# Kernel tuning notes

Measured on AMD Instinct MI355X. Metric: run time of the kernel, lower is better.

## Reference

```python
import jax, jax.numpy as jnp
import numpy as np

B, NQ, NK, D, H, DR, MLPD = 32, 32, 4096, 256, 8, 2, 2048
ID = D // DR  # internal dim for downsampled cross-attention
EPS = 1e-5


def _ln(x, g, b):
    m = jnp.mean(x, -1, keepdims=True)
    v = jnp.mean((x - m) ** 2, -1, keepdims=True)
    return (x - m) / jnp.sqrt(v + EPS) * g + b


def _attn(q, k, v, qw, qb, kw, kb, vw, vb, ow, ob):
    # linear projections (weights stored as [in, out])
    q = q @ qw + qb
    k = k @ kw + kb
    v = v @ vw + vb
    b, nq, c = q.shape
    d = c // H
    qh = q.reshape(b, nq, H, d)
    kh = k.reshape(b, -1, H, d)
    vh = v.reshape(b, -1, H, d)
    scores = jnp.einsum('bqhd,bkhd->bhqk', qh, kh) * (1.0 / np.sqrt(d))
    a = jax.nn.softmax(scores, axis=-1)
    o = jnp.einsum('bhqk,bkhd->bqhd', a, vh).reshape(b, nq, c)
    return o @ ow + ob


def _forward(queries, keys, query_pe,
             sa_qw, sa_qb, sa_kw, sa_kb, sa_vw, sa_vb, sa_ow, sa_ob,
             t2i_qw, t2i_qb, t2i_kw, t2i_kb, t2i_vw, t2i_vb, t2i_ow, t2i_ob,
             i2t_qw, i2t_qb, i2t_kw, i2t_kb, i2t_vw, i2t_vb, i2t_ow, i2t_ob,
             mlp_w1, mlp_b1, mlp_w2, mlp_b2,
             ln1_g, ln1_b, ln2_g, ln2_b, ln3_g, ln3_b, ln4_g, ln4_b):
    # skip_first_layer_pe = False
    queries = queries + query_pe
    attn_out = _attn(queries, queries, queries,
                     sa_qw, sa_qb, sa_kw, sa_kb, sa_vw, sa_vb, sa_ow, sa_ob)
    queries = _ln(queries + attn_out, ln1_g, ln1_b)
    # cross attention: tokens -> image
    q = queries + query_pe
    attn_out = _attn(q, keys, keys,
                     t2i_qw, t2i_qb, t2i_kw, t2i_kb, t2i_vw, t2i_vb, t2i_ow, t2i_ob)
    queries = _ln(queries + attn_out, ln2_g, ln2_b)
    # MLP block (num_layers=1): act(x W1 + b1) W2 + b2, act = ReLU
    mlp_out = jax.nn.relu(queries @ mlp_w1 + mlp_b1) @ mlp_w2 + mlp_b2
    queries = _ln(queries + mlp_out, ln3_g, ln3_b)
    # cross attention: image -> tokens
    q = queries + query_pe
    attn_out = _attn(keys, q, queries,
                     i2t_qw, i2t_qb, i2t_kw, i2t_kb, i2t_vw, i2t_vb, i2t_ow, i2t_ob)
    keys = _ln(keys + attn_out, ln4_g, ln4_b)
    return queries, keys


def setup_inputs() -> dict:
    key = jax.random.key(0)
    ks = iter(jax.random.split(key, 64))
    def w(shape, s=0.02):
        return jax.random.normal(next(ks), shape, jnp.float32) * s
    inp = {
        'queries': w((B, NQ, D), 1.0),
        'keys': w((B, NK, D), 1.0),
        'query_pe': w((B, NQ, D), 1.0),
    }
    for pre, idim in [('sa', D), ('t2i', ID), ('i2t', ID)]:
        inp[pre + '_qw'] = w((D, idim)); inp[pre + '_qb'] = jnp.zeros((idim,), jnp.float32)
        inp[pre + '_kw'] = w((D, idim)); inp[pre + '_kb'] = jnp.zeros((idim,), jnp.float32)
        inp[pre + '_vw'] = w((D, idim)); inp[pre + '_vb'] = jnp.zeros((idim,), jnp.float32)
        inp[pre + '_ow'] = w((idim, D)); inp[pre + '_ob'] = jnp.zeros((D,), jnp.float32)
    inp['mlp_w1'] = w((D, MLPD)); inp['mlp_b1'] = jnp.zeros((MLPD,), jnp.float32)
    inp['mlp_w2'] = w((MLPD, D)); inp['mlp_b2'] = jnp.zeros((D,), jnp.float32)
    for i in range(1, 5):
        inp['ln%d_g' % i] = jnp.ones((D,), jnp.float32)
        inp['ln%d_b' % i] = jnp.zeros((D,), jnp.float32)
    return inp


def reference(queries, keys, query_pe,
              sa_qw, sa_qb, sa_kw, sa_kb, sa_vw, sa_vb, sa_ow, sa_ob,
              t2i_qw, t2i_qb, t2i_kw, t2i_kb, t2i_vw, t2i_vb, t2i_ow, t2i_ob,
              i2t_qw, i2t_qb, i2t_kw, i2t_kb, i2t_vw, i2t_vb, i2t_ow, i2t_ob,
              mlp_w1, mlp_b1, mlp_w2, mlp_b2,
              ln1_g, ln1_b, ln2_g, ln2_b, ln3_g, ln3_b, ln4_g, ln4_b):
    return _forward(queries, keys, query_pe,
                    sa_qw, sa_qb, sa_kw, sa_kb, sa_vw, sa_vb, sa_ow, sa_ob,
                    t2i_qw, t2i_qb, t2i_kw, t2i_kb, t2i_vw, t2i_vb, t2i_ow, t2i_ob,
                    i2t_qw, i2t_qb, i2t_kw, i2t_kb, i2t_vw, i2t_vb, i2t_ow, i2t_ob,
                    mlp_w1, mlp_b1, mlp_w2, mlp_b2,
                    ln1_g, ln1_b, ln2_g, ln2_b, ln3_g, ln3_b, ln4_g, ln4_b)
```

## Files before the change

kernel.cpp:

```cpp
#include <hip/hip_runtime.h>

typedef unsigned short u16;
typedef __attribute__((ext_vector_type(8))) short s16x8;
typedef __attribute__((ext_vector_type(4))) float f32x4;
typedef __attribute__((ext_vector_type(8))) unsigned short u16x8;

__device__ __forceinline__ float b2f(u16 u) {
  union { unsigned int i; float f; } v; v.i = ((unsigned int)u) << 16; return v.f;
}
__device__ __forceinline__ u16 f2b(float f) {
  union { float f; unsigned int i; } v; v.f = f;
  unsigned int r = v.i + 0x7FFFu + ((v.i >> 16) & 1u);
  return (u16)(r >> 16);
}
__device__ __forceinline__ int pk2(float a, float b) {
  return (int)f2b(a) | ((int)f2b(b) << 16);
}

template<bool RELU>
__global__ void __launch_bounds__(256) k_gemm(
    const u16* __restrict__ A, const u16* __restrict__ Wt,
    const float* __restrict__ bias, u16* __restrict__ C, int N, int K)
{
  __shared__ int4 smem4[2048];
  char* AsB = (char*)smem4;
  char* WsB = (char*)smem4 + 16384;
  const int t = threadIdx.x;
  const int lane = t & 63, wid = t >> 6;
  const int wm = wid >> 1, wn = wid & 1;
  const int l16 = lane & 15, lhi = lane >> 4;
  const int bCol = blockIdx.x * 128;
  const int bRow = blockIdx.y * 128;

  f32x4 acc[4][4];
#pragma unroll
  for (int i = 0; i < 4; ++i)
#pragma unroll
    for (int j = 0; j < 4; ++j) acc[i][j] = (f32x4){0.f, 0.f, 0.f, 0.f};

  const int nk = K >> 6;
  for (int kt = 0; kt < nk; ++kt) {
    const int k0 = kt << 6;
    int4 av[4], wv[4];
#pragma unroll
    for (int i = 0; i < 4; ++i) {
      int L = i * 4096 + t * 16;
      int r = L >> 7, cl = (L >> 4) & 7;
      av[i] = *(const int4*)(A + (size_t)(bRow + r) * K + k0 + cl * 8);
      wv[i] = *(const int4*)(Wt + (size_t)(bCol + r) * K + k0 + cl * 8);
    }
    if (kt) __syncthreads();
#pragma unroll
    for (int i = 0; i < 4; ++i) {
      int L = i * 4096 + t * 16;
      int r = L >> 7, cl = (L >> 4) & 7;
      int off = r * 128 + ((cl ^ (r & 7)) << 4);
      *(int4*)(AsB + off) = av[i];
      *(int4*)(WsB + off) = wv[i];
    }
    __syncthreads();
#pragma unroll
    for (int kk = 0; kk < 2; ++kk) {
      s16x8 af[4], bfr[4];
#pragma unroll
      for (int mt = 0; mt < 4; ++mt) {
        int r = wm * 64 + mt * 16 + l16;
        int ch = kk * 4 + lhi;
        af[mt] = *(const s16x8*)(AsB + r * 128 + ((ch ^ (r & 7)) << 4));
      }
#pragma unroll
      for (int nt = 0; nt < 4; ++nt) {
        int r = wn * 64 + nt * 16 + l16;
        int ch = kk * 4 + lhi;
        bfr[nt] = *(const s16x8*)(WsB + r * 128 + ((ch ^ (r & 7)) << 4));
      }
#pragma unroll
      for (int mt = 0; mt < 4; ++mt)
#pragma unroll
        for (int nt = 0; nt < 4; ++nt)
          acc[mt][nt] = __builtin_amdgcn_mfma_f32_16x16x32_bf16(
              af[mt], bfr[nt], acc[mt][nt], 0, 0, 0);
    }
  }
#pragma unroll
  for (int mt = 0; mt < 4; ++mt) {
#pragma unroll
    for (int nt = 0; nt < 4; ++nt) {
      int cg = bCol + wn * 64 + nt * 16 + l16;
      float bv = bias[cg];
#pragma unroll
      for (int rg = 0; rg < 4; ++rg) {
        int rgl = bRow + wm * 64 + mt * 16 + lhi * 4 + rg;
        float v = acc[mt][nt][rg] + bv;
        if (RELU) v = fmaxf(v, 0.f);
        C[(size_t)rgl * N + cg] = f2b(v);
      }
    }
  }
}

__global__ void __launch_bounds__(512, 2) k_gemm_kvq(
    const float* __restrict__ A, const u16* __restrict__ Wt,
    const float* __restrict__ bias, u16* __restrict__ KV, u16* __restrict__ QB)
{
  __shared__ char smem[49152];
  char* AsB = smem;
  const int t = threadIdx.x;
  const int lane = t & 63, wid = t >> 6;
  const int wm = wid >> 2, wn = wid & 3;
  const int l16 = lane & 15, lhi = lane >> 4;
  const int bRow = blockIdx.x * 128;

  f32x4 acc[4][6];
#pragma unroll
  for (int i = 0; i < 4; ++i)
#pragma unroll
    for (int j = 0; j < 6; ++j) acc[i][j] = (f32x4){0.f, 0.f, 0.f, 0.f};

  for (int kt = 0; kt < 4; ++kt) {
    const int k0 = kt << 6;
    float4 a0r[2], a1r[2];
#pragma unroll
    for (int i = 0; i < 2; ++i) {
      int L = i * 8192 + t * 16;
      int r = L >> 7, cl = (L >> 4) & 7;
      const float* Af = A + (size_t)(bRow + r) * 256 + k0 + cl * 8;
      a0r[i] = *(const float4*)Af;
      a1r[i] = *(const float4*)(Af + 4);
    }
    if (kt) __syncthreads();
#pragma unroll
    for (int i = 0; i < 2; ++i) {
      int L = i * 8192 + t * 16;
      int r = L >> 7, cl = (L >> 4) & 7;
      int4 p = (int4){pk2(a0r[i].x, a0r[i].y), pk2(a0r[i].z, a0r[i].w),
                      pk2(a1r[i].x, a1r[i].y), pk2(a1r[i].z, a1r[i].w)};
      *(int4*)(AsB + r * 128 + ((cl ^ (r & 7)) << 4)) = p;
    }
    __syncthreads();
#pragma unroll
    for (int kk = 0; kk < 2; ++kk) {
      s16x8 af[4], bfr[6];
#pragma unroll
      for (int nt = 0; nt < 6; ++nt) {
        int row = wn * 96 + nt * 16 + l16;
        bfr[nt] = *(const s16x8*)(Wt + (size_t)row * 256 + k0 + kk * 32 + lhi * 8);
      }
#pragma unroll
      for (int mt = 0; mt < 4; ++mt) {
        int r = wm * 64 + mt * 16 + l16;
        int ch = kk * 4 + lhi;
        af[mt] = *(const s16x8*)(AsB + r * 128 + ((ch ^ (r & 7)) << 4));
      }
#pragma unroll
      for (int mt = 0; mt < 4; ++mt)
#pragma unroll
        for (int nt = 0; nt < 6; ++nt)
          acc[mt][nt] = __builtin_amdgcn_mfma_f32_16x16x32_bf16(
              af[mt], bfr[nt], acc[mt][nt], 0, 0, 0);
    }
  }
  u16* ldsO = (u16*)smem;
  for (int half = 0; half < 2; ++half) {
    __syncthreads();
    if (wm == half) {
#pragma unroll
      for (int mt = 0; mt < 4; ++mt) {
#pragma unroll
        for (int nt = 0; nt < 6; ++nt) {
          int cg = wn * 96 + nt * 16 + l16;
          float bv = bias[cg];
#pragma unroll
          for (int rg = 0; rg < 4; ++rg) {
            int r = mt * 16 + lhi * 4 + rg;
            ldsO[r * 384 + cg] = f2b(acc[mt][nt][rg] + bv);
          }
        }
      }
    }
    __syncthreads();
#pragma unroll
    for (int i = 0; i < 6; ++i) {
      int chunk = i * 512 + t;
      int r = chunk / 48, c8 = chunk - r * 48;
      int row = bRow + half * 64 + r;
      int4 v = *(int4*)(ldsO + r * 384 + c8 * 8);
      if (c8 < 32) *(int4*)(KV + (size_t)row * 256 + c8 * 8) = v;
      else         *(int4*)(QB + (size_t)row * 128 + (c8 - 32) * 8) = v;
    }
  }
}

__global__ void __launch_bounds__(256) k_gemm_ln(
    const u16* __restrict__ A, const u16* __restrict__ Wt,
    const float* __restrict__ bias, const float* __restrict__ res,
    const float* __restrict__ g, const float* __restrict__ bl,
    float* __restrict__ out)
{
  __shared__ int4 smem4[512];
  __shared__ float rsum[2][32][2], rsq[2][32][2];
  char* AsB = (char*)smem4;
  const int t = threadIdx.x;
  const int lane = t & 63, wid = t >> 6;
  const int wm = wid >> 1, wn = wid & 1;
  const int l16 = lane & 15, lhi = lane >> 4;
  const int bRow = blockIdx.x * 64;

  f32x4 acc[2][8];
#pragma unroll
  for (int i = 0; i < 2; ++i)
#pragma unroll
    for (int j = 0; j < 8; ++j) acc[i][j] = (f32x4){0.f, 0.f, 0.f, 0.f};

  for (int kt = 0; kt < 2; ++kt) {
    const int k0 = kt << 6;
    int4 av[2];
#pragma unroll
    for (int i = 0; i < 2; ++i) {
      int L = i * 4096 + t * 16;
      int r = L >> 7, cl = (L >> 4) & 7;
      av[i] = *(const int4*)(A + (size_t)(bRow + r) * 128 + k0 + cl * 8);
    }
    if (kt) __syncthreads();
#pragma unroll
    for (int i = 0; i < 2; ++i) {
      int L = i * 4096 + t * 16;
      int r = L >> 7, cl = (L >> 4) & 7;
      *(int4*)(AsB + r * 128 + ((cl ^ (r & 7)) << 4)) = av[i];
    }
    __syncthreads();
#pragma unroll
    for (int kk = 0; kk < 2; ++kk) {
      s16x8 af[2], bfr[8];
#pragma unroll
      for (int nt = 0; nt < 8; ++nt) {
        int row = wn * 128 + nt * 16 + l16;
        bfr[nt] = *(const s16x8*)(Wt + (size_t)row * 128 + k0 + kk * 32 + lhi * 8);
      }
#pragma unroll
      for (int mt = 0; mt < 2; ++mt) {
        int r = wm * 32 + mt * 16 + l16;
        int ch = kk * 4 + lhi;
        af[mt] = *(const s16x8*)(AsB + r * 128 + ((ch ^ (r & 7)) << 4));
      }
#pragma unroll
      for (int mt = 0; mt < 2; ++mt)
#pragma unroll
        for (int nt = 0; nt < 8; ++nt)
          acc[mt][nt] = __builtin_amdgcn_mfma_f32_16x16x32_bf16(
              af[mt], bfr[nt], acc[mt][nt], 0, 0, 0);
    }
  }
#pragma unroll
  for (int mt = 0; mt < 2; ++mt) {
#pragma unroll
    for (int nt = 0; nt < 8; ++nt) {
      int cg = wn * 128 + nt * 16 + l16;
      float bv = bias[cg];
#pragma unroll
      for (int rg = 0; rg < 4; ++rg) {
        int row = bRow + wm * 32 + mt * 16 + lhi * 4 + rg;
        acc[mt][nt][rg] += bv + res[(size_t)row * 256 + cg];
      }
    }
  }
#pragma unroll
  for (int mt = 0; mt < 2; ++mt) {
#pragma unroll
    for (int rg = 0; rg < 4; ++rg) {
      float ps = 0.f, pq = 0.f;
#pragma unroll
      for (int nt = 0; nt < 8; ++nt) {
        float v = acc[mt][nt][rg];
        ps += v; pq += v * v;
      }
#pragma unroll
      for (int msk = 1; msk < 16; msk <<= 1) {
        ps += __shfl_xor(ps, msk);
        pq += __shfl_xor(pq, msk);
      }
      if (l16 == 0) {
        int rl = mt * 16 + lhi * 4 + rg;
        rsum[wm][rl][wn] = ps;
        rsq[wm][rl][wn] = pq;
      }
    }
  }
  __syncthreads();
#pragma unroll
  for (int mt = 0; mt < 2; ++mt) {
#pragma unroll
    for (int rg = 0; rg < 4; ++rg) {
      int rl = mt * 16 + lhi * 4 + rg;
      float ts = rsum[wm][rl][0] + rsum[wm][rl][1];
      float tq = rsq[wm][rl][0] + rsq[wm][rl][1];
      float mean = ts * (1.f / 256.f);
      float var = tq * (1.f / 256.f) - mean * mean;
      float rstd = rsqrtf(var + 1e-5f);
      int row = bRow + wm * 32 + rl;
#pragma unroll
      for (int nt = 0; nt < 8; ++nt) {
        int cg = wn * 128 + nt * 16 + l16;
        out[(size_t)row * 256 + cg] =
            (acc[mt][nt][rg] - mean) * rstd * g[cg] + bl[cg];
      }
    }
  }
}

struct TDesc { const float* src; void* dst; int K; int N; int mode; int blk0; };
struct TArgs { TDesc d[24]; int n; };

__global__ void __launch_bounds__(256) k_trans(TArgs a)
{
  int blk = blockIdx.x;
  int i = 0;
  while (i + 1 < a.n && blk >= a.d[i + 1].blk0) ++i;
  TDesc td = a.d[i];
  int e = (blk - td.blk0) * 256 + threadIdx.x;
  int tot = td.K * td.N;
  if (e >= tot) return;
  if (td.mode == 0) {
    int k = e / td.N, n = e - k * td.N;
    ((u16*)td.dst)[(size_t)n * td.K + k] = f2b(td.src[e]);
  } else {
    ((float*)td.dst)[e] = td.src[e];
  }
}

__global__ void __launch_bounds__(256) k_addpe(
    const float* __restrict__ q, const float* __restrict__ pe,
    float* __restrict__ outf, u16* __restrict__ outb)
{
  int i = blockIdx.x * 256 + threadIdx.x;
  float v = q[i] + pe[i];
  outf[i] = v;
  outb[i] = f2b(v);
}

__global__ void __launch_bounds__(64) k_attn_sa(
    const u16* __restrict__ QKV, u16* __restrict__ out)
{
  __shared__ float Q[32][33], K[32][33], V[32][33];
  int b = blockIdx.x >> 3, h = blockIdx.x & 7;
  int t = threadIdx.x;
  for (int idx = t; idx < 1024; idx += 64) {
    int i = idx >> 5, d = idx & 31;
    size_t base = (size_t)(b * 32 + i) * 768 + h * 32 + d;
    Q[i][d] = b2f(QKV[base]);
    K[i][d] = b2f(QKV[base + 256]);
    V[i][d] = b2f(QKV[base + 512]);
  }
  __syncthreads();
  int i = t & 31, half = t >> 5;
  float s[16];
#pragma unroll
  for (int jj = 0; jj < 16; ++jj) {
    int j = half * 16 + jj;
    float a = 0.f;
#pragma unroll
    for (int d = 0; d < 32; ++d) a += Q[i][d] * K[j][d];
    s[jj] = a * 0.17677669529663687f;
  }
  float m = s[0];
#pragma unroll
  for (int jj = 1; jj < 16; ++jj) m = fmaxf(m, s[jj]);
  m = fmaxf(m, __shfl_xor(m, 32));
  float sum = 0.f;
#pragma unroll
  for (int jj = 0; jj < 16; ++jj) { s[jj] = __expf(s[jj] - m); sum += s[jj]; }
  sum += __shfl_xor(sum, 32);
  float o[32];
#pragma unroll
  for (int d = 0; d < 32; ++d) o[d] = 0.f;
#pragma unroll
  for (int jj = 0; jj < 16; ++jj) {
    int j = half * 16 + jj;
    float p = s[jj];
#pragma unroll
    for (int d = 0; d < 32; ++d) o[d] += p * V[j][d];
  }
  float inv = 1.f / sum;
#pragma unroll
  for (int d = 0; d < 32; ++d) {
    float v = o[d] + __shfl_xor(o[d], 32);
    if (half == 0) out[(size_t)(b * 32 + i) * 256 + h * 32 + d] = f2b(v * inv);
  }
}

__global__ void __launch_bounds__(128) k_attn_t2i_part(
    const u16* __restrict__ Qt, const u16* __restrict__ KV,
    float* __restrict__ part)
{
  __shared__ int4 kvs[4096];
  int c = blockIdx.x, b = blockIdx.y;
  int tid = threadIdx.x;
  const int4* src = (const int4*)(KV + ((size_t)b * 4096 + c * 128) * 256);
  for (int i = tid; i < 4096; i += 128) kvs[i] = src[i];
  __syncthreads();
  int qp = tid >> 3, h = tid & 7;
  const u16* lds = (const u16*)kvs;

  float q0[16], q1[16];
  {
    const u16* p0 = Qt + (size_t)(b * 32 + qp) * 128 + h * 16;
    const u16* p1 = Qt + (size_t)(b * 32 + qp + 16) * 128 + h * 16;
    u16x8 a0 = *(const u16x8*)p0, b0 = *(const u16x8*)(p0 + 8);
    u16x8 a1 = *(const u16x8*)p1, b1 = *(const u16x8*)(p1 + 8);
#pragma unroll
    for (int e = 0; e < 8; ++e) {
      q0[e] = b2f(a0[e]); q0[8 + e] = b2f(b0[e]);
      q1[e] = b2f(a1[e]); q1[8 + e] = b2f(b1[e]);
    }
  }
  float m0 = -INFINITY, s0 = 0.f, m1 = -INFINITY, s1 = 0.f;
  float acc0[16], acc1[16];
#pragma unroll
  for (int d = 0; d < 16; ++d) { acc0[d] = 0.f; acc1[d] = 0.f; }

  for (int j = 0; j < 128; ++j) {
    const u16* kr = lds + j * 256 + h * 16;
    u16x8 ka = *(const u16x8*)kr;
    u16x8 kb = *(const u16x8*)(kr + 8);
    float l0 = 0.f, l1 = 0.f;
#pragma unroll
    for (int e = 0; e < 8; ++e) {
      float klo = b2f(ka[e]), khi = b2f(kb[e]);
      l0 += q0[e] * klo + q0[8 + e] * khi;
      l1 += q1[e] * klo + q1[8 + e] * khi;
    }
    l0 *= 0.25f; l1 *= 0.25f;
    const u16* vr = kr + 128;
    u16x8 va = *(const u16x8*)vr;
    u16x8 vb = *(const u16x8*)(vr + 8);
    float nm0 = fmaxf(m0, l0), nm1 = fmaxf(m1, l1);
    float c0 = __expf(m0 - nm0), p0 = __expf(l0 - nm0);
    float c1 = __expf(m1 - nm1), p1 = __expf(l1 - nm1);
    s0 = s0 * c0 + p0; s1 = s1 * c1 + p1;
#pragma unroll
    for (int e = 0; e < 8; ++e) {
      float vlo = b2f(va[e]), vhi = b2f(vb[e]);
      acc0[e] = acc0[e] * c0 + p0 * vlo;
      acc0[8 + e] = acc0[8 + e] * c0 + p0 * vhi;
      acc1[e] = acc1[e] * c1 + p1 * vlo;
      acc1[8 + e] = acc1[8 + e] * c1 + p1 * vhi;
    }
    m0 = nm0; m1 = nm1;
  }
  float* r0 = part + (((size_t)(b * 32 + qp) * 8 + h) * 32 + c) * 18;
  float* r1 = part + (((size_t)(b * 32 + qp + 16) * 8 + h) * 32 + c) * 18;
#pragma unroll
  for (int d = 0; d < 16; ++d) { r0[d] = acc0[d]; r1[d] = acc1[d]; }
  r0[16] = m0; r0[17] = s0;
  r1[16] = m1; r1[17] = s1;
}

__global__ void __launch_bounds__(256) k_attn_t2i_merge(
    const float* __restrict__ part, u16* __restrict__ out)
{
  int b = blockIdx.x >> 3, h = blockIdx.x & 7;
  int q = threadIdx.x >> 3, ds = threadIdx.x & 7;
  const float* base = part + (((size_t)(b * 32 + q) * 8 + h) * 32) * 18;
  float mg = -INFINITY;
#pragma unroll 4
  for (int c = 0; c < 32; ++c) mg = fmaxf(mg, base[c * 18 + 16]);
  float sg = 0.f, a0 = 0.f, a1 = 0.f;
#pragma unroll 4
  for (int c = 0; c < 32; ++c) {
    const float* rec = base + c * 18;
    float w = __expf(rec[16] - mg);
    sg += rec[17] * w;
    a0 += rec[ds * 2] * w;
    a1 += rec[ds * 2 + 1] * w;
  }
  float inv = 1.f / sg;
  u16* op = out + (size_t)(b * 32 + q) * 128 + h * 16 + ds * 2;
  op[0] = f2b(a0 * inv);
  op[1] = f2b(a1 * inv);
}

__global__ void __launch_bounds__(256) k_attn_i2t(
    const u16* __restrict__ Qb, const u16* __restrict__ Kc,
    const u16* __restrict__ Vc, u16* __restrict__ out)
{
  __shared__ float Kl[32][132], Vl[32][132];
  int blk = blockIdx.x;
  int b = blk >> 7;
  int r0 = (blk & 127) * 32;
  for (int idx = threadIdx.x; idx < 4096; idx += 256) {
    int j = idx >> 7, c = idx & 127;
    Kl[j][c] = b2f(Kc[(size_t)(b * 32 + j) * 128 + c]);
    Vl[j][c] = b2f(Vc[(size_t)(b * 32 + j) * 128 + c]);
  }
  __syncthreads();
  int lr = threadIdx.x >> 3, h = threadIdx.x & 7;
  size_t row = (size_t)b * 4096 + r0 + lr;
  const u16* qp = Qb + row * 128 + h * 16;
  float q[16];
  {
    u16x8 qa = *(const u16x8*)qp;
    u16x8 qb2 = *(const u16x8*)(qp + 8);
#pragma unroll
    for (int e = 0; e < 8; ++e) { q[e] = b2f(qa[e]); q[8 + e] = b2f(qb2[e]); }
  }
  float lg[32];
  float mx = -INFINITY;
#pragma unroll
  for (int j = 0; j < 32; ++j) {
    float a = 0.f;
#pragma unroll
    for (int d = 0; d < 16; ++d) a += q[d] * Kl[j][h * 16 + d];
    lg[j] = a * 0.25f;
    mx = fmaxf(mx, lg[j]);
  }
  float sum = 0.f;
#pragma unroll
  for (int j = 0; j < 32; ++j) { lg[j] = __expf(lg[j] - mx); sum += lg[j]; }
  float acc[16];
#pragma unroll
  for (int d = 0; d < 16; ++d) acc[d] = 0.f;
#pragma unroll
  for (int j = 0; j < 32; ++j) {
    float p = lg[j];
#pragma unroll
    for (int d = 0; d < 16; ++d) acc[d] += p * Vl[j][h * 16 + d];
  }
  float inv = 1.f / sum;
  u16* op = out + row * 128 + h * 16;
#pragma unroll
  for (int d = 0; d < 16; ++d) op[d] = f2b(acc[d] * inv);
}

__global__ void __launch_bounds__(256) k_addln_small(
    const float* __restrict__ res, const u16* __restrict__ delta,
    const float* __restrict__ g, const float* __restrict__ bb,
    float* outf, u16* outb, const float* pe, u16* outpe)
{
  int row = blockIdx.x * 4 + (threadIdx.x >> 6);
  int lane = threadIdx.x & 63;
  size_t base = (size_t)row * 256 + lane * 4;
  float4 xv = *(const float4*)(res + base);
  ushort4 dv = *(const ushort4*)(delta + base);
  float v0 = xv.x + b2f(dv.x), v1 = xv.y + b2f(dv.y);
  float v2 = xv.z + b2f(dv.z), v3 = xv.w + b2f(dv.w);
  float sum = v0 + v1 + v2 + v3;
  float sq = v0 * v0 + v1 * v1 + v2 * v2 + v3 * v3;
#pragma unroll
  for (int msk = 1; msk < 64; msk <<= 1) {
    sum += __shfl_xor(sum, msk);
    sq += __shfl_xor(sq, msk);
  }
  float mean = sum * (1.f / 256.f);
  float var = sq * (1.f / 256.f) - mean * mean;
  float rstd = rsqrtf(var + 1e-5f);
  float4 gv = *(const float4*)(g + lane * 4);
  float4 bv = *(const float4*)(bb + lane * 4);
  float y0 = (v0 - mean) * rstd * gv.x + bv.x;
  float y1 = (v1 - mean) * rstd * gv.y + bv.y;
  float y2 = (v2 - mean) * rstd * gv.z + bv.z;
  float y3 = (v3 - mean) * rstd * gv.w + bv.w;
  if (outf) { float4 o{y0, y1, y2, y3}; *(float4*)(outf + base) = o; }
  if (outb) {
    ushort4 o{f2b(y0), f2b(y1), f2b(y2), f2b(y3)};
    *(ushort4*)(outb + base) = o;
  }
  if (outpe) {
    float4 pv = *(const float4*)(pe + base);
    ushort4 o{f2b(y0 + pv.x), f2b(y1 + pv.y), f2b(y2 + pv.z), f2b(y3 + pv.w)};
    *(ushort4*)(outpe + base) = o;
  }
}

extern "C" void kernel_launch(void* const* d_in, const int* in_sizes, int n_in,
                              void* d_out, int out_size, void* d_ws, size_t ws_size,
                              hipStream_t stream)
{
  (void)in_sizes; (void)n_in; (void)out_size; (void)ws_size;
  const float* queries = (const float*)d_in[0];
  const float* keys    = (const float*)d_in[1];
  const float* qpe     = (const float*)d_in[2];
  const float* sa_qw = (const float*)d_in[3];  const float* sa_qb = (const float*)d_in[4];
  const float* sa_kw = (const float*)d_in[5];  const float* sa_kb = (const float*)d_in[6];
  const float* sa_vw = (const float*)d_in[7];  const float* sa_vb = (const float*)d_in[8];
  const float* sa_ow = (const float*)d_in[9];  const float* sa_ob = (const float*)d_in[10];
  const float* t2i_qw = (const float*)d_in[11]; const float* t2i_qb = (const float*)d_in[12];
  const float* t2i_kw = (const float*)d_in[13]; const float* t2i_kb = (const float*)d_in[14];
  const float* t2i_vw = (const float*)d_in[15]; const float* t2i_vb = (const float*)d_in[16];
  const float* t2i_ow = (const float*)d_in[17]; const float* t2i_ob = (const float*)d_in[18];
  const float* i2t_qw = (const float*)d_in[19]; const float* i2t_qb = (const float*)d_in[20];
  const float* i2t_kw = (const float*)d_in[21]; const float* i2t_kb = (const float*)d_in[22];
  const float* i2t_vw = (const float*)d_in[23]; const float* i2t_vb = (const float*)d_in[24];
  const float* i2t_ow = (const float*)d_in[25]; const float* i2t_ob = (const float*)d_in[26];
  const float* mlp_w1 = (const float*)d_in[27]; const float* mlp_b1 = (const float*)d_in[28];
  const float* mlp_w2 = (const float*)d_in[29]; const float* mlp_b2 = (const float*)d_in[30];
  const float* ln1_g = (const float*)d_in[31]; const float* ln1_b = (const float*)d_in[32];
  const float* ln2_g = (const float*)d_in[33]; const float* ln2_b = (const float*)d_in[34];
  const float* ln3_g = (const float*)d_in[35]; const float* ln3_b = (const float*)d_in[36];
  const float* ln4_g = (const float*)d_in[37]; const float* ln4_b = (const float*)d_in[38];

  float* out_q = (float*)d_out;
  float* out_k = out_q + 262144;

  u16* kvbuf  = (u16*)out_k;
  u16* qb_big = (u16*)out_k + 33554432;
  float* t2i_part = (float*)((u16*)out_k + 50331648);

  char* ws = (char*)d_ws;
  size_t off = 0;
  auto alloc = [&](size_t bytes) -> char* {
    char* p = ws + off;
    off += (bytes + 255) & ~(size_t)255;
    return p;
  };
  u16* wt_saqkv = (u16*)alloc(768 * 256 * 2);
  u16* wt_saow  = (u16*)alloc(256 * 256 * 2);
  u16* wt_t2iq  = (u16*)alloc(128 * 256 * 2);
  u16* wt_kvq   = (u16*)alloc(384 * 256 * 2);
  u16* wt_t2io  = (u16*)alloc(256 * 128 * 2);
  u16* wt_i2tk  = (u16*)alloc(128 * 256 * 2);
  u16* wt_i2tv  = (u16*)alloc(128 * 256 * 2);
  u16* wt_i2to  = (u16*)alloc(256 * 128 * 2);
  u16* wt_w1    = (u16*)alloc(2048 * 256 * 2);
  u16* wt_w2    = (u16*)alloc(256 * 2048 * 2);
  float* b_saqkv = (float*)alloc(768 * 4);
  float* b_kvq   = (float*)alloc(384 * 4);
  float* q0f = (float*)alloc(262144 * 4);
  float* q1f = (float*)alloc(262144 * 4);
  float* q2f = (float*)alloc(262144 * 4);
  u16* q0b   = (u16*)alloc(262144 * 2);
  u16* qkvs  = (u16*)alloc(786432 * 2);
  u16* attn1 = (u16*)alloc(262144 * 2);
  u16* o1    = (u16*)alloc(262144 * 2);
  u16* q1pe  = (u16*)alloc(262144 * 2);
  u16* qt    = (u16*)alloc(131072 * 2);
  u16* at2   = (u16*)alloc(131072 * 2);
  u16* o2    = (u16*)alloc(262144 * 2);
  u16* q2b   = (u16*)alloc(262144 * 2);
  u16* hbuf  = (u16*)alloc(2097152 * 2);
  u16* mo    = (u16*)alloc(262144 * 2);
  u16* q3b   = (u16*)alloc(262144 * 2);
  u16* q3pe  = (u16*)alloc(262144 * 2);
  u16* kc    = (u16*)alloc(131072 * 2);
  u16* vc    = (u16*)alloc(131072 * 2);
  u16* ab_big = (u16*)alloc((size_t)16777216 * 2);

  TArgs ta{};
  int nb = 0, id = 0;
  auto addT = [&](const float* s, void* d, int K, int N, int mode) {
    ta.d[id].src = s; ta.d[id].dst = d; ta.d[id].K = K; ta.d[id].N = N;
    ta.d[id].mode = mode; ta.d[id].blk0 = nb;
    nb += (K * N + 255) / 256;
    ++id;
  };
  addT(sa_qw, wt_saqkv, 256, 256, 0);
  addT(sa_kw, wt_saqkv + 256 * 256, 256, 256, 0);
  addT(sa_vw, wt_saqkv + 512 * 256, 256, 256, 0);
  addT(sa_ow, wt_saow, 256, 256, 0);
  addT(t2i_qw, wt_t2iq, 256, 128, 0);
  addT(t2i_kw, wt_kvq, 256, 128, 0);
  addT(t2i_vw, wt_kvq + 128 * 256, 256, 128, 0);
  addT(i2t_qw, wt_kvq + 256 * 256, 256, 128, 0);
  addT(t2i_ow, wt_t2io, 128, 256, 0);
  addT(i2t_kw, wt_i2tk, 256, 128, 0);
  addT(i2t_vw, wt_i2tv, 256, 128, 0);
  addT(i2t_ow, wt_i2to, 128, 256, 0);
  addT(mlp_w1, wt_w1, 256, 2048, 0);
  addT(mlp_w2, wt_w2, 2048, 256, 0);
  addT(sa_qb, b_saqkv, 1, 256, 1);
  addT(sa_kb, b_saqkv + 256, 1, 256, 1);
  addT(sa_vb, b_saqkv + 512, 1, 256, 1);
  addT(t2i_kb, b_kvq, 1, 128, 1);
  addT(t2i_vb, b_kvq + 128, 1, 128, 1);
  addT(i2t_qb, b_kvq + 256, 1, 128, 1);
  ta.n = id;
  k_trans<<<nb, 256, 0, stream>>>(ta);

  k_addpe<<<1024, 256, 0, stream>>>(queries, qpe, q0f, q0b);
  k_gemm<false><<<dim3(6, 8), 256, 0, stream>>>(q0b, wt_saqkv, b_saqkv,
                                                qkvs, 768, 256);
  k_attn_sa<<<256, 64, 0, stream>>>(qkvs, attn1);
  k_gemm<false><<<dim3(2, 8), 256, 0, stream>>>(attn1, wt_saow, sa_ob,
                                                o1, 256, 256);
  k_addln_small<<<256, 256, 0, stream>>>(q0f, o1, ln1_g, ln1_b, q1f, nullptr,
                                         qpe, q1pe);
  k_gemm<false><<<dim3(1, 8), 256, 0, stream>>>(q1pe, wt_t2iq, t2i_qb,
                                                qt, 128, 256);
  k_gemm_kvq<<<1024, 512, 0, stream>>>(keys, wt_kvq, b_kvq, kvbuf, qb_big);
  k_attn_t2i_part<<<dim3(32, 32), 128, 0, stream>>>(qt, kvbuf, t2i_part);
  k_attn_t2i_merge<<<256, 256, 0, stream>>>(t2i_part, at2);
  k_gemm<false><<<dim3(2, 8), 256, 0, stream>>>(at2, wt_t2io, t2i_ob,
                                                o2, 256, 128);
  k_addln_small<<<256, 256, 0, stream>>>(q1f, o2, ln2_g, ln2_b, q2f, q2b,
                                         nullptr, nullptr);
  k_gemm<true><<<dim3(16, 8), 256, 0, stream>>>(q2b, wt_w1, mlp_b1,
                                                hbuf, 2048, 256);
  k_gemm<false><<<dim3(2, 8), 256, 0, stream>>>(hbuf, wt_w2, mlp_b2,
                                                mo, 256, 2048);
  k_addln_small<<<256, 256, 0, stream>>>(q2f, mo, ln3_g, ln3_b, out_q, q3b,
                                         qpe, q3pe);
  k_gemm<false><<<dim3(1, 8), 256, 0, stream>>>(q3pe, wt_i2tk, i2t_kb,
                                                kc, 128, 256);
  k_gemm<false><<<dim3(1, 8), 256, 0, stream>>>(q3b, wt_i2tv, i2t_vb,
                                                vc, 128, 256);
  k_attn_i2t<<<4096, 256, 0, stream>>>(qb_big, kc, vc, ab_big);
  k_gemm_ln<<<2048, 256, 0, stream>>>(ab_big, wt_i2to, i2t_ob, keys,
                                      ln4_g, ln4_b, out_k);
}
```

Measured before the change: 574.0 us.

## Fuse query-side self-attention, out-proj, LayerNorm and t2i Q projection into one kernel

Replaces six launches (add-PE, QKV GEMM, self-attention, out-proj GEMM, add+LayerNorm, t2i Q GEMM) with one kernel that has one block per batch and keeps intermediates in LDS. This removes launch overhead and global round-trips for the small query-side tensors. The trade-off is only 32 blocks on the GPU, with each block streaming all the weights from global/L2, so parallelism is lower. LayerNorm now uses a single-pass variance (E[x^2]-mean^2).

```diff
diff --git a/kernel.cpp b/kernel.cpp
--- a/kernel.cpp
+++ b/kernel.cpp
@@ -96,6 +96,239 @@
         C[(size_t)rgl * N + cg] = f2b(v);
       }
     }
+  }
+}
+
+__global__ void __launch_bounds__(256) k_qphase1(
+    const float* __restrict__ queries, const float* __restrict__ qpe,
+    const u16* __restrict__ Wqkv,
+    const float* __restrict__ bqkv,
+    const u16* __restrict__ Wo,
+    const float* __restrict__ ob,
+    const float* __restrict__ g1, const float* __restrict__ b1,
+    const u16* __restrict__ Wq2,
+    const float* __restrict__ qb2,
+    float* __restrict__ q1f, u16* __restrict__ qt)
+{
+  __shared__ float q0f[32][260];
+  __shared__ u16 qkv[32][776];
+  __shared__ u16 atb[32][264];
+  __shared__ float rs[32][4], rq[32][4];
+  const int b = blockIdx.x;
+  const int t = threadIdx.x;
+  const int lane = t & 63, w = t >> 6;
+  const int l16 = lane & 15, lhi = lane >> 4;
+
+  {
+    const float4* qg = (const float4*)(queries + (size_t)b * 8192);
+    const float4* pg = (const float4*)(qpe + (size_t)b * 8192);
+    for (int i = t; i < 2048; i += 256) {
+      int row = i >> 6, c4 = (i & 63) * 4;
+      float4 qv = qg[i], pv = pg[i];
+      *(float4*)&q0f[row][c4] =
+          (float4){qv.x + pv.x, qv.y + pv.y, qv.z + pv.z, qv.w + pv.w};
+    }
+  }
+  __syncthreads();
+
+  {
+    f32x4 acc[2][12];
+#pragma unroll
+    for (int i = 0; i < 2; ++i)
+#pragma unroll
+      for (int j = 0; j < 12; ++j) acc[i][j] = (f32x4){0.f, 0.f, 0.f, 0.f};
+#pragma unroll
+    for (int kk = 0; kk < 8; ++kk) {
+      const int ko = kk * 32 + lhi * 8;
+      s16x8 af[2], bfr[12];
+#pragma unroll
+      for (int mt = 0; mt < 2; ++mt) {
+        const float* ap = &q0f[mt * 16 + l16][ko];
+        float4 x = *(const float4*)ap;
+        float4 y = *(const float4*)(ap + 4);
+        int4 p = (int4){pk2(x.x, x.y), pk2(x.z, x.w),
+                        pk2(y.x, y.y), pk2(y.z, y.w)};
+        af[mt] = *(s16x8*)&p;
+      }
+#pragma unroll
+      for (int nt = 0; nt < 12; ++nt) {
+        int row = w * 192 + nt * 16 + l16;
+        bfr[nt] = *(const s16x8*)(Wqkv + (size_t)row * 256 + ko);
+      }
+#pragma unroll
+      for (int mt = 0; mt < 2; ++mt)
+#pragma unroll
+        for (int nt = 0; nt < 12; ++nt)
+          acc[mt][nt] = __builtin_amdgcn_mfma_f32_16x16x32_bf16(
+              af[mt], bfr[nt], acc[mt][nt], 0, 0, 0);
+    }
+#pragma unroll
+    for (int mt = 0; mt < 2; ++mt)
+#pragma unroll
+      for (int nt = 0; nt < 12; ++nt) {
+        int cg = w * 192 + nt * 16 + l16;
+        float bv = bqkv[cg];
+#pragma unroll
+        for (int rg = 0; rg < 4; ++rg)
+          qkv[mt * 16 + lhi * 4 + rg][cg] = f2b(acc[mt][nt][rg] + bv);
+      }
+  }
+  __syncthreads();
+
+  {
+    int q = t >> 3, h = t & 7;
+    float Qh[32];
+#pragma unroll
+    for (int c = 0; c < 4; ++c) {
+      u16x8 v = *(const u16x8*)&qkv[q][h * 32 + c * 8];
+#pragma unroll
+      for (int e = 0; e < 8; ++e) Qh[c * 8 + e] = b2f(v[e]);
+    }
+    float s[32], mx = -INFINITY;
+#pragma unroll 4
+    for (int j = 0; j < 32; ++j) {
+      float a = 0.f;
+#pragma unroll
+      for (int c = 0; c < 4; ++c) {
+        u16x8 v = *(const u16x8*)&qkv[j][256 + h * 32 + c * 8];
+#pragma unroll
+        for (int e = 0; e < 8; ++e) a += Qh[c * 8 + e] * b2f(v[e]);
+      }
+      s[j] = a * 0.17677669529663687f;
+      mx = fmaxf(mx, s[j]);
+    }
+    float sum = 0.f;
+#pragma unroll
+    for (int j = 0; j < 32; ++j) { s[j] = __expf(s[j] - mx); sum += s[j]; }
+    float o[32];
+#pragma unroll
+    for (int d = 0; d < 32; ++d) o[d] = 0.f;
+#pragma unroll 4
+    for (int j = 0; j < 32; ++j) {
+      float p = s[j];
+#pragma unroll
+      for (int c = 0; c < 4; ++c) {
+        u16x8 v = *(const u16x8*)&qkv[j][512 + h * 32 + c * 8];
+#pragma unroll
+        for (int e = 0; e < 8; ++e) o[c * 8 + e] += p * b2f(v[e]);
+      }
+    }
+    float inv = 1.f / sum;
+#pragma unroll
+    for (int d = 0; d < 32; ++d) atb[q][h * 32 + d] = f2b(o[d] * inv);
+  }
+  __syncthreads();
+
+  float yv[2][4][4];
+  {
+    f32x4 acc[2][4];
+#pragma unroll
+    for (int i = 0; i < 2; ++i)
+#pragma unroll
+      for (int j = 0; j < 4; ++j) acc[i][j] = (f32x4){0.f, 0.f, 0.f, 0.f};
+#pragma unroll
+    for (int kk = 0; kk < 8; ++kk) {
+      const int ko = kk * 32 + lhi * 8;
+      s16x8 af[2], bfr[4];
+#pragma unroll
+      for (int mt = 0; mt < 2; ++mt)
+        af[mt] = *(const s16x8*)&atb[mt * 16 + l16][ko];
+#pragma unroll
+      for (int nt = 0; nt < 4; ++nt) {
+        int row = w * 64 + nt * 16 + l16;
+        bfr[nt] = *(const s16x8*)(Wo + (size_t)row * 256 + ko);
+      }
+#pragma unroll
+      for (int mt = 0; mt < 2; ++mt)
+#pragma unroll
+        for (int nt = 0; nt < 4; ++nt)
+          acc[mt][nt] = __builtin_amdgcn_mfma_f32_16x16x32_bf16(
+              af[mt], bfr[nt], acc[mt][nt], 0, 0, 0);
+    }
+#pragma unroll
+    for (int mt = 0; mt < 2; ++mt) {
+#pragma unroll
+      for (int rg = 0; rg < 4; ++rg) {
+        int row = mt * 16 + lhi * 4 + rg;
+        float ps = 0.f, pq = 0.f;
+#pragma unroll
+        for (int nt = 0; nt < 4; ++nt) {
+          int cg = w * 64 + nt * 16 + l16;
+          float v = acc[mt][nt][rg] + ob[cg] + q0f[row][cg];
+          yv[mt][nt][rg] = v;
+          ps += v; pq += v * v;
+        }
+#pragma unroll
+        for (int msk = 1; msk < 16; msk <<= 1) {
+          ps += __shfl_xor(ps, msk);
+          pq += __shfl_xor(pq, msk);
+        }
+        if (l16 == 0) { rs[row][w] = ps; rq[row][w] = pq; }
+      }
+    }
+  }
+  __syncthreads();
+  {
+#pragma unroll
+    for (int mt = 0; mt < 2; ++mt) {
+#pragma unroll
+      for (int rg = 0; rg < 4; ++rg) {
+        int row = mt * 16 + lhi * 4 + rg;
+        float ts = rs[row][0] + rs[row][1] + rs[row][2] + rs[row][3];
+        float tq = rq[row][0] + rq[row][1] + rq[row][2] + rq[row][3];
+        float mean = ts * (1.f / 256.f);
+        float var = tq * (1.f / 256.f) - mean * mean;
+        float rstd = rsqrtf(var + 1e-5f);
+#pragma unroll
+        for (int nt = 0; nt < 4; ++nt) {
+          int cg = w * 64 + nt * 16 + l16;
+          float y = (yv[mt][nt][rg] - mean) * rstd * g1[cg] + b1[cg];
+          size_t gi = ((size_t)b * 32 + row) * 256 + cg;
+          q1f[gi] = y;
+          atb[row][cg] = f2b(y + qpe[gi]);
+        }
+      }
+    }
+  }
+  __syncthreads();
+
+  {
+    f32x4 acc[2][2];
+#pragma unroll
+    for (int i = 0; i < 2; ++i)
+#pragma unroll
+      for (int j = 0; j < 2; ++j) acc[i][j] = (f32x4){0.f, 0.f, 0.f, 0.f};
+#pragma unroll
+    for (int kk = 0; kk < 8; ++kk) {
+      const int ko = kk * 32 + lhi * 8;
+      s16x8 af[2], bfr[2];
+#pragma unroll
+      for (int mt = 0; mt < 2; ++mt)
+        af[mt] = *(const s16x8*)&atb[mt * 16 + l16][ko];
+#pragma unroll
+      for (int nt = 0; nt < 2; ++nt) {
+        int row = w * 32 + nt * 16 + l16;
+        bfr[nt] = *(const s16x8*)(Wq2 + (size_t)row * 256 + ko);
+      }
+#pragma unroll
+      for (int mt = 0; mt < 2; ++mt)
+#pragma unroll
+        for (int nt = 0; nt < 2; ++nt)
+          acc[mt][nt] = __builtin_amdgcn_mfma_f32_16x16x32_bf16(
+              af[mt], bfr[nt], acc[mt][nt], 0, 0, 0);
+    }
+#pragma unroll
+    for (int mt = 0; mt < 2; ++mt)
+#pragma unroll
+      for (int nt = 0; nt < 2; ++nt) {
+        int cg = w * 32 + nt * 16 + l16;
+        float bv = qb2[cg];
+#pragma unroll
+        for (int rg = 0; rg < 4; ++rg) {
+          int row = mt * 16 + lhi * 4 + rg;
+          qt[((size_t)b * 32 + row) * 128 + cg] = f2b(acc[mt][nt][rg] + bv);
+        }
+      }
   }
 }
 
@@ -325,66 +558,6 @@
     ((u16*)td.dst)[(size_t)n * td.K + k] = f2b(td.src[e]);
   } else {
     ((float*)td.dst)[e] = td.src[e];
-  }
-}
-
-__global__ void __launch_bounds__(256) k_addpe(
-    const float* __restrict__ q, const float* __restrict__ pe,
-    float* __restrict__ outf, u16* __restrict__ outb)
-{
-  int i = blockIdx.x * 256 + threadIdx.x;
-  float v = q[i] + pe[i];
-  outf[i] = v;
-  outb[i] = f2b(v);
-}
-
-__global__ void __launch_bounds__(64) k_attn_sa(
-    const u16* __restrict__ QKV, u16* __restrict__ out)
-{
-  __shared__ float Q[32][33], K[32][33], V[32][33];
-  int b = blockIdx.x >> 3, h = blockIdx.x & 7;
-  int t = threadIdx.x;
-  for (int idx = t; idx < 1024; idx += 64) {
-    int i = idx >> 5, d = idx & 31;
-    size_t base = (size_t)(b * 32 + i) * 768 + h * 32 + d;
-    Q[i][d] = b2f(QKV[base]);
-    K[i][d] = b2f(QKV[base + 256]);
-    V[i][d] = b2f(QKV[base + 512]);
-  }
-  __syncthreads();
-  int i = t & 31, half = t >> 5;
-  float s[16];
-#pragma unroll
-  for (int jj = 0; jj < 16; ++jj) {
-    int j = half * 16 + jj;
-    float a = 0.f;
-#pragma unroll
-    for (int d = 0; d < 32; ++d) a += Q[i][d] * K[j][d];
-    s[jj] = a * 0.17677669529663687f;
-  }
-  float m = s[0];
-#pragma unroll
-  for (int jj = 1; jj < 16; ++jj) m = fmaxf(m, s[jj]);
-  m = fmaxf(m, __shfl_xor(m, 32));
-  float sum = 0.f;
-#pragma unroll
-  for (int jj = 0; jj < 16; ++jj) { s[jj] = __expf(s[jj] - m); sum += s[jj]; }
-  sum += __shfl_xor(sum, 32);
-  float o[32];
-#pragma unroll
-  for (int d = 0; d < 32; ++d) o[d] = 0.f;
-#pragma unroll
-  for (int jj = 0; jj < 16; ++jj) {
-    int j = half * 16 + jj;
-    float p = s[jj];
-#pragma unroll
-    for (int d = 0; d < 32; ++d) o[d] += p * V[j][d];
-  }
-  float inv = 1.f / sum;
-#pragma unroll
-  for (int d = 0; d < 32; ++d) {
-    float v = o[d] + __shfl_xor(o[d], 32);
-    if (half == 0) out[(size_t)(b * 32 + i) * 256 + h * 32 + d] = f2b(v * inv);
   }
 }
 
@@ -624,14 +797,8 @@
   u16* wt_w2    = (u16*)alloc(256 * 2048 * 2);
   float* b_saqkv = (float*)alloc(768 * 4);
   float* b_kvq   = (float*)alloc(384 * 4);
-  float* q0f = (float*)alloc(262144 * 4);
   float* q1f = (float*)alloc(262144 * 4);
   float* q2f = (float*)alloc(262144 * 4);
-  u16* q0b   = (u16*)alloc(262144 * 2);
-  u16* qkvs  = (u16*)alloc(786432 * 2);
-  u16* attn1 = (u16*)alloc(262144 * 2);
-  u16* o1    = (u16*)alloc(262144 * 2);
-  u16* q1pe  = (u16*)alloc(262144 * 2);
   u16* qt    = (u16*)alloc(131072 * 2);
   u16* at2   = (u16*)alloc(131072 * 2);
   u16* o2    = (u16*)alloc(262144 * 2);
@@ -675,16 +842,9 @@
   ta.n = id;
   k_trans<<<nb, 256, 0, stream>>>(ta);
 
-  k_addpe<<<1024, 256, 0, stream>>>(queries, qpe, q0f, q0b);
-  k_gemm<false><<<dim3(6, 8), 256, 0, stream>>>(q0b, wt_saqkv, b_saqkv,
-                                                qkvs, 768, 256);
-  k_attn_sa<<<256, 64, 0, stream>>>(qkvs, attn1);
-  k_gemm<false><<<dim3(2, 8), 256, 0, stream>>>(attn1, wt_saow, sa_ob,
-                                                o1, 256, 256);
-  k_addln_small<<<256, 256, 0, stream>>>(q0f, o1, ln1_g, ln1_b, q1f, nullptr,
-                                         qpe, q1pe);
-  k_gemm<false><<<dim3(1, 8), 256, 0, stream>>>(q1pe, wt_t2iq, t2i_qb,
-                                                qt, 128, 256);
+  k_qphase1<<<32, 256, 0, stream>>>(queries, qpe, wt_saqkv, b_saqkv,
+                                    wt_saow, sa_ob, ln1_g, ln1_b,
+                                    wt_t2iq, t2i_qb, q1f, qt);
   k_gemm_kvq<<<1024, 512, 0, stream>>>(keys, wt_kvq, b_kvq, kvbuf, qb_big);
   k_attn_t2i_part<<<dim3(32, 32), 128, 0, stream>>>(qt, kvbuf, t2i_part);
   k_attn_t2i_merge<<<256, 256, 0, stream>>>(t2i_part, at2);
```

Result: faster. 550.9 us (-4.0%).
